# Optimization experiments

Hardware: AMD Instinct MI355X
Metric: run time of the kernel (lower is better)

## Reference

```python
import jax, jax.numpy as jnp
import numpy as np

LN_EPS = 1e-5
NEG_SLOPE = 0.01  # torch LeakyReLU default


def layernorm(x, w, b):
    m = jnp.mean(x, axis=-1, keepdims=True)
    v = jnp.mean((x - m) ** 2, axis=-1, keepdims=True)
    return (x - m) * jax.lax.rsqrt(v + LN_EPS) * w + b


def setup_inputs() -> dict:
    key = jax.random.key(0)
    ks = jax.random.split(key, 12)
    B, T, C, E = 16, 1024, 768, 2
    d = C
    s = 0.02
    inp = {
        "x": jax.random.normal(ks[0], (B, T, C), jnp.float32),
        "ln1_w": jnp.ones((C,), jnp.float32),
        "ln1_b": jnp.zeros((C,), jnp.float32),
        "wqkv": jax.random.normal(ks[1], (C, 3 * C), jnp.float32) * s,
        "bqkv": jnp.zeros((3 * C,), jnp.float32),
        "wproj": jax.random.normal(ks[2], (C, C), jnp.float32) * s,
        "bproj": jnp.zeros((C,), jnp.float32),
        "ln2_w": jnp.ones((C,), jnp.float32),
        "ln2_b": jnp.zeros((C,), jnp.float32),
        "wg": jax.random.normal(ks[3], (C, E), jnp.float32) * s,
        # Experts module uses torch.randn (std 1); we scale down for numerics
        "w1": jax.random.normal(ks[4], (E, d, 4 * d), jnp.float32) * s,
        "w2": jax.random.normal(ks[5], (E, 4 * d, 4 * d), jnp.float32) * s,
        "w3": jax.random.normal(ks[6], (E, 4 * d, d), jnp.float32) * s,
        "n_head": 12,
    }
    return inp


def block_forward(x, ln1_w, ln1_b, wqkv, bqkv, wproj, bproj,
                  ln2_w, ln2_b, wg, w1, w2, w3, n_head):
    B, T, C = x.shape
    H = n_head
    hd = C // H
    E = wg.shape[-1]

    # ---- causal self-attention + residual ----
    h = layernorm(x, ln1_w, ln1_b)
    qkv = h @ wqkv + bqkv                      # [B,T,3C]
    q, k, v = jnp.split(qkv, 3, axis=-1)
    q = q.reshape(B, T, H, hd).transpose(0, 2, 1, 3)  # bhtd
    k = k.reshape(B, T, H, hd).transpose(0, 2, 1, 3)
    v = v.reshape(B, T, H, hd).transpose(0, 2, 1, 3)
    scores = jnp.einsum('bhqd,bhkd->bhqk', q, k) / jnp.sqrt(jnp.float32(hd))
    causal = jnp.tril(jnp.ones((T, T), bool))
    scores = jnp.where(causal, scores, jnp.finfo(scores.dtype).min)
    attn = jax.nn.softmax(scores, axis=-1)
    y = jnp.einsum('bhqk,bhkd->bhqd', attn, v)
    y = y.transpose(0, 2, 1, 3).reshape(B, T, C)
    x = x + (y @ wproj + bproj)

    # ---- MoE (top-2 gating, capacity dispatch) + residual ----
    h2 = layernorm(x, ln2_w, ln2_b)
    capacity = (T * 2) // E                    # capacity_factor = 1.0, top-2
    raw_gates = jax.nn.softmax(h2 @ wg, axis=-1)   # [B,T,E]

    idx1 = jnp.argmax(raw_gates, axis=-1)
    mask1 = jax.nn.one_hot(idx1, E, dtype=raw_gates.dtype)
    gate1 = jnp.sum(raw_gates * mask1, axis=-1)    # [B,T]
    gates2 = raw_gates * (1.0 - mask1)
    idx2 = jnp.argmax(gates2, axis=-1)
    mask2 = jax.nn.one_hot(idx2, E, dtype=raw_gates.dtype)
    gate2 = jnp.sum(raw_gates * mask2, axis=-1)
    denom = gate1 + gate2 + 1e-9
    gate1, gate2 = gate1 / denom, gate2 / denom

    # aux load-balancing loss (before capacity truncation)
    density = jnp.mean(mask1, axis=1)              # [B,E]
    density_proxy = jnp.mean(raw_gates, axis=1)    # [B,E]
    aux_loss = jnp.mean(density * density_proxy) * (E * E)

    # positions within each expert buffer (exclusive cumsum over tokens)
    pos1 = jnp.cumsum(mask1, axis=1) - mask1       # [B,T,E]
    mask1 = mask1 * (pos1 < capacity)
    mask1_count = jnp.sum(mask1, axis=1, keepdims=True)
    pos2 = (jnp.cumsum(mask2, axis=1) - mask2) + mask1_count
    mask2 = mask2 * (pos2 < capacity)

    oh1 = jax.nn.one_hot(pos1.astype(jnp.int32), capacity, dtype=raw_gates.dtype)
    oh2 = jax.nn.one_hot(pos2.astype(jnp.int32), capacity, dtype=raw_gates.dtype)
    combine = (gate1[..., None] * mask1)[..., None] * oh1 \
            + (gate2[..., None] * mask2)[..., None] * oh2   # [B,T,E,C]
    dispatch = (combine > 0).astype(h2.dtype)

    # dispatch -> per-expert batches
    expert_in = jnp.einsum('bnd,bnec->ebcd', h2, dispatch)   # [E,B,Cap,d]
    Bc = B * capacity
    ei = expert_in.reshape(E, Bc, C)
    lrelu = lambda z: jnp.where(z >= 0, z, NEG_SLOPE * z)
    hh = lrelu(jnp.einsum('end,edh->enh', ei, w1))
    hh = lrelu(jnp.einsum('end,edh->enh', hh, w2))
    eo = jnp.einsum('end,edh->enh', hh, w3).reshape(E, B, capacity, C)
    moe_out = jnp.einsum('ebcd,bnec->bnd', eo, combine)

    x = x + moe_out
    return x, aux_loss


def reference(x, ln1_w, ln1_b, wqkv, bqkv, wproj, bproj,
              ln2_w, ln2_b, wg, w1, w2, w3, n_head):
    return block_forward(x, ln1_w, ln1_b, wqkv, bqkv, wproj, bproj,
                         ln2_w, ln2_b, wg, w1, w2, w3, n_head)
```

## Files before the change

### kernel.cpp

```cpp
#include <hip/hip_runtime.h>
#include <cstdint>
#include <cstddef>

constexpr int B_  = 16;
constexpr int T_  = 1024;
constexpr int C_  = 768;
constexpr int H_  = 12;
constexpr int HD_ = 64;
constexpr int BT_ = B_ * T_;
constexpr int C3_ = 3 * C_;
constexpr int FF_ = 4 * C_;
constexpr int MCH_ = 8192;

typedef __bf16 bf16x8 __attribute__((ext_vector_type(8)));
typedef float  floatx4 __attribute__((ext_vector_type(4)));
typedef unsigned short u16x8 __attribute__((ext_vector_type(8)));

__device__ inline float bf2f(unsigned short u) {
  union { unsigned int i; float f; } x; x.i = ((unsigned int)u) << 16; return x.f;
}
__device__ inline unsigned short f2bf(float f) {
  union { float f; unsigned int i; } x; x.f = f;
  unsigned int u = x.i;
  u += 0x7fffu + ((u >> 16) & 1u);
  return (unsigned short)(u >> 16);
}

#define GLOAD_LDS16(gp, lp)                                              \
  __builtin_amdgcn_global_load_lds(                                      \
      (__attribute__((address_space(1))) void*)(gp),                     \
      (__attribute__((address_space(3))) void*)(lp), 16, 0, 0)

__launch_bounds__(256)
__global__ void ln_kernel(const float* __restrict__ x, const float* __restrict__ w,
                          const float* __restrict__ b, unsigned short* __restrict__ out) {
  int row = blockIdx.x;
  int tid = threadIdx.x;
  const float* xr = x + (size_t)row * C_;
  float v0 = xr[tid], v1 = xr[tid + 256], v2 = xr[tid + 512];
  float s  = v0 + v1 + v2;
  float ss = v0 * v0 + v1 * v1 + v2 * v2;
#pragma unroll
  for (int off = 32; off > 0; off >>= 1) {
    s  += __shfl_down(s, off, 64);
    ss += __shfl_down(ss, off, 64);
  }
  __shared__ float red[8];
  int wid = tid >> 6;
  if ((tid & 63) == 0) { red[wid] = s; red[4 + wid] = ss; }
  __syncthreads();
  float st  = red[0] + red[1] + red[2] + red[3];
  float sst = red[4] + red[5] + red[6] + red[7];
  float mean = st * (1.0f / C_);
  float var  = sst * (1.0f / C_) - mean * mean;
  float rstd = rsqrtf(var + 1e-5f);
  unsigned short* orow = out + (size_t)row * C_;
  orow[tid]       = f2bf((v0 - mean) * rstd * w[tid]       + b[tid]);
  orow[tid + 256] = f2bf((v1 - mean) * rstd * w[tid + 256] + b[tid + 256]);
  orow[tid + 512] = f2bf((v2 - mean) * rstd * w[tid + 512] + b[tid + 512]);
}

__launch_bounds__(256)
__global__ void convT(const float* __restrict__ in, unsigned short* __restrict__ out,
                      int K, int N) {
  __shared__ float t[32][33];
  int n0 = blockIdx.x * 32, k0 = blockIdx.y * 32;
  int tx = threadIdx.x & 31, ty = threadIdx.x >> 5;
#pragma unroll
  for (int r = 0; r < 32; r += 8)
    t[r + ty][tx] = in[(size_t)(k0 + r + ty) * N + n0 + tx];
  __syncthreads();
#pragma unroll
  for (int r = 0; r < 32; r += 8)
    out[(size_t)(n0 + r + ty) * K + k0 + tx] = f2bf(t[tx][r + ty]);
}

template <int ACT, bool BIAS, bool RES, bool COMBINE, bool OUTBF16>
__launch_bounds__(256)
__global__ void gemm_bf16(const unsigned short* __restrict__ A,
                          const unsigned short* __restrict__ Bt,
                          const float* __restrict__ bias,
                          const float* __restrict__ Rres,
                          const float* __restrict__ gates2, int eidx,
                          void* __restrict__ Cout,
                          int M, int N, int K) {
  __shared__ __attribute__((aligned(16))) unsigned short Als[8192];
  __shared__ __attribute__((aligned(16))) unsigned short Bls[8192];
  const int tid  = threadIdx.x;
  const int wave = tid >> 6, lane = tid & 63;
  const int wr = wave >> 1, wc = wave & 1;
  const int m0 = blockIdx.y * 128, n0 = blockIdx.x * 128;

  const int srow = wave * 32 + (lane >> 3);
  const int skg  = (lane & 7) ^ ((lane >> 3) & 7);
  const unsigned short* Ap = A  + (size_t)(m0 + srow) * K + skg * 8;
  const unsigned short* Bp = Bt + (size_t)(n0 + srow) * K + skg * 8;
  unsigned short* AlsW = Als + wave * 2048;
  unsigned short* BlsW = Bls + wave * 2048;

  floatx4 acc[4][4];
#pragma unroll
  for (int i = 0; i < 4; ++i)
#pragma unroll
    for (int j = 0; j < 4; ++j) acc[i][j] = floatx4{0.f, 0.f, 0.f, 0.f};

  const int q  = lane >> 4;
  const int ml = lane & 15;
  const int rsw = ml & 7;

  for (int k0 = 0; k0 < K; k0 += 64) {
    __syncthreads();
#pragma unroll
    for (int i = 0; i < 4; ++i) {
      GLOAD_LDS16(Ap + (size_t)(i * 8) * K + k0, AlsW + i * 512);
      GLOAD_LDS16(Bp + (size_t)(i * 8) * K + k0, BlsW + i * 512);
    }
    __syncthreads();
#pragma unroll
    for (int ks = 0; ks < 2; ++ks) {
      const int p = (ks * 4 + q) ^ rsw;
      bf16x8 af[4], bfg[4];
#pragma unroll
      for (int i = 0; i < 4; ++i) {
        int ar = wr * 64 + i * 16 + ml;
        af[i]  = *(const bf16x8*)&Als[(ar * 8 + p) * 8];
        int br = wc * 64 + i * 16 + ml;
        bfg[i] = *(const bf16x8*)&Bls[(br * 8 + p) * 8];
      }
#pragma unroll
      for (int i = 0; i < 4; ++i)
#pragma unroll
        for (int j = 0; j < 4; ++j)
          acc[i][j] = __builtin_amdgcn_mfma_f32_16x16x32_bf16(af[i], bfg[j], acc[i][j], 0, 0, 0);
    }
  }

  const int rbase = q * 4;
#pragma unroll
  for (int i = 0; i < 4; ++i) {
    int row = m0 + wr * 64 + i * 16 + rbase;
#pragma unroll
    for (int j = 0; j < 4; ++j) {
      int col = n0 + wc * 64 + j * 16 + ml;
      float bcol = BIAS ? bias[col] : 0.f;
#pragma unroll
      for (int r = 0; r < 4; ++r) {
        float v = acc[i][j][r];
        if (BIAS) v += bcol;
        if (ACT == 1) v = (v >= 0.f) ? v : 0.01f * v;
        if (RES) v += Rres[(size_t)(row + r) * N + col];
        if (COMBINE) {
          float g = gates2[2 * (row + r) + eidx];
          float* op = (float*)Cout + (size_t)(row + r) * N + col;
          *op += g * v;
        } else if (OUTBF16) {
          ((unsigned short*)Cout)[(size_t)(row + r) * N + col] = f2bf(v);
        } else {
          ((float*)Cout)[(size_t)(row + r) * N + col] = v;
        }
      }
    }
  }
}

__launch_bounds__(256)
__global__ void attn_kernel(const unsigned short* __restrict__ qkv,
                            unsigned short* __restrict__ y) {
  __shared__ __attribute__((aligned(16))) unsigned short Qls[64 * 64];
  __shared__ __attribute__((aligned(16))) unsigned short Kls[64 * 64];
  __shared__ __attribute__((aligned(16))) unsigned short Vt[64 * 72];
  __shared__ __attribute__((aligned(16))) unsigned short Pls[4 * 16 * 72];

  const int tid  = threadIdx.x;
  const int wave = tid >> 6, lane = tid & 63;
  const int quad = lane >> 4, n = lane & 15;
  const int q0 = blockIdx.x * 64;
  const int bh = blockIdx.y;
  const int b = bh / H_, h = bh % H_;
  const size_t base = (size_t)b * T_ * C3_ + (size_t)h * HD_;

  {
    const int r8 = lane >> 3;
    const int g  = (lane & 7) ^ r8;
#pragma unroll
    for (int i = 0; i < 2; ++i) {
      int row = wave * 16 + i * 8 + r8;
      GLOAD_LDS16(qkv + base + (size_t)(q0 + row) * C3_ + g * 8,
                  Qls + wave * 1024 + i * 512);
    }
  }

  floatx4 O[4];
#pragma unroll
  for (int ct = 0; ct < 4; ++ct) O[ct] = floatx4{0.f, 0.f, 0.f, 0.f};
  float mrow[4] = {-1e30f, -1e30f, -1e30f, -1e30f};
  float lrow[4] = {0.f, 0.f, 0.f, 0.f};

  const int nkt = blockIdx.x + 1;
  unsigned short* Pw = Pls + wave * (16 * 72);

  for (int kt = 0; kt < nkt; ++kt) {
    const int k0 = kt << 6;
    __syncthreads();
    {
      const int r8 = lane >> 3;
      const int g  = (lane & 7) ^ r8;
#pragma unroll
      for (int i = 0; i < 2; ++i) {
        int key = wave * 16 + i * 8 + r8;
        GLOAD_LDS16(qkv + base + (size_t)(k0 + key) * C3_ + C_ + g * 8,
                    Kls + wave * 1024 + i * 512);
      }
    }
    {
      int key = tid & 63;
      int dbase = (tid >> 6) * 8;
#pragma unroll
      for (int it = 0; it < 2; ++it) {
        int d0 = dbase + it * 32;
        u16x8 vv = *(const u16x8*)(qkv + base + (size_t)(k0 + key) * C3_ + 2 * C_ + d0);
#pragma unroll
        for (int j = 0; j < 8; ++j) Vt[(d0 + j) * 72 + key] = vv[j];
      }
    }
    __syncthreads();

    floatx4 sacc[4];
#pragma unroll
    for (int ct = 0; ct < 4; ++ct) sacc[ct] = floatx4{0.f, 0.f, 0.f, 0.f};
#pragma unroll
    for (int ks = 0; ks < 2; ++ks) {
      const int ga = (ks * 4 + quad) ^ (n & 7);
      bf16x8 aq = *(const bf16x8*)&Qls[((wave * 16 + n) * 8 + ga) * 8];
#pragma unroll
      for (int ct = 0; ct < 4; ++ct) {
        bf16x8 kb = *(const bf16x8*)&Kls[((ct * 16 + n) * 8 + ga) * 8];
        sacc[ct] = __builtin_amdgcn_mfma_f32_16x16x32_bf16(aq, kb, sacc[ct], 0, 0, 0);
      }
    }

    float p[4][4];
#pragma unroll
    for (int ct = 0; ct < 4; ++ct)
#pragma unroll
      for (int r = 0; r < 4; ++r) p[ct][r] = sacc[ct][r] * 0.125f;
    if (kt == nkt - 1) {
      const int kgb = k0 + n, qgb = q0 + wave * 16 + quad * 4;
#pragma unroll
      for (int ct = 0; ct < 4; ++ct)
#pragma unroll
        for (int r = 0; r < 4; ++r)
          if (kgb + ct * 16 > qgb + r) p[ct][r] = -1e30f;
    }
#pragma unroll
    for (int r = 0; r < 4; ++r) {
      float tm = fmaxf(fmaxf(p[0][r], p[1][r]), fmaxf(p[2][r], p[3][r]));
      tm = fmaxf(tm, __shfl_xor(tm, 1, 64));
      tm = fmaxf(tm, __shfl_xor(tm, 2, 64));
      tm = fmaxf(tm, __shfl_xor(tm, 4, 64));
      tm = fmaxf(tm, __shfl_xor(tm, 8, 64));
      float mn = fmaxf(mrow[r], tm);
      float alpha = __expf(mrow[r] - mn);
      mrow[r] = mn;
      float ps = 0.f;
#pragma unroll
      for (int ct = 0; ct < 4; ++ct) {
        float pe = __expf(p[ct][r] - mn);
        p[ct][r] = pe;
        ps += pe;
      }
      ps += __shfl_xor(ps, 1, 64);
      ps += __shfl_xor(ps, 2, 64);
      ps += __shfl_xor(ps, 4, 64);
      ps += __shfl_xor(ps, 8, 64);
      lrow[r] = lrow[r] * alpha + ps;
      O[0][r] *= alpha; O[1][r] *= alpha; O[2][r] *= alpha; O[3][r] *= alpha;
    }

#pragma unroll
    for (int ct = 0; ct < 4; ++ct)
#pragma unroll
      for (int r = 0; r < 4; ++r)
        Pw[(quad * 4 + r) * 72 + ct * 16 + n] = f2bf(p[ct][r]);

#pragma unroll
    for (int ks = 0; ks < 2; ++ks) {
      bf16x8 pa = *(const bf16x8*)&Pw[n * 72 + (ks * 4 + quad) * 8];
#pragma unroll
      for (int ct = 0; ct < 4; ++ct) {
        bf16x8 vb = *(const bf16x8*)&Vt[(ct * 16 + n) * 72 + (ks * 4 + quad) * 8];
        O[ct] = __builtin_amdgcn_mfma_f32_16x16x32_bf16(pa, vb, O[ct], 0, 0, 0);
      }
    }
  }

#pragma unroll
  for (int r = 0; r < 4; ++r) {
    float inv = 1.0f / lrow[r];
    int row = q0 + wave * 16 + quad * 4 + r;
    unsigned short* dst = y + ((size_t)b * T_ + row) * C_ + h * HD_;
#pragma unroll
    for (int ct = 0; ct < 4; ++ct)
      dst[ct * 16 + n] = f2bf(O[ct][r] * inv);
  }
}

__launch_bounds__(256)
__global__ void gate_kernel(const unsigned short* __restrict__ h2,
                            const float* __restrict__ wg,
                            float* __restrict__ gates) {
  int wave = threadIdx.x >> 6, lane = threadIdx.x & 63;
  int t = blockIdx.x * 4 + wave;
  const unsigned short* hr = h2 + (size_t)t * C_;
  float a0 = 0.0f, a1 = 0.0f;
#pragma unroll
  for (int i = 0; i < 12; ++i) {
    int d = lane + 64 * i;
    float hv = bf2f(hr[d]);
    a0 += hv * wg[2 * d];
    a1 += hv * wg[2 * d + 1];
  }
#pragma unroll
  for (int off = 32; off > 0; off >>= 1) {
    a0 += __shfl_down(a0, off, 64);
    a1 += __shfl_down(a1, off, 64);
  }
  if (lane == 0) {
    float m  = fmaxf(a0, a1);
    float e0 = __expf(a0 - m), e1 = __expf(a1 - m);
    float invs = 1.0f / (e0 + e1);
    float p0 = e0 * invs, p1 = e1 * invs;
    const float gnorm = 1.0f / (1.0f + 1e-9f);
    gates[2 * t]     = p0 * gnorm;
    gates[2 * t + 1] = p1 * gnorm;
  }
}

__launch_bounds__(1024)
__global__ void moe_stats_kernel(const float* __restrict__ gates,
                                 float* __restrict__ out_aux) {
  int wave = threadIdx.x >> 6, lane = threadIdx.x & 63;
  float c0 = 0.f, sp0 = 0.f, sp1 = 0.f;
#pragma unroll
  for (int j = 0; j < 16; ++j) {
    int t = wave * T_ + lane + 64 * j;
    float p0 = gates[2 * t], p1 = gates[2 * t + 1];
    c0  += (p1 > p0) ? 0.f : 1.f;
    sp0 += p0;
    sp1 += p1;
  }
#pragma unroll
  for (int off = 32; off > 0; off >>= 1) {
    c0  += __shfl_down(c0, off, 64);
    sp0 += __shfl_down(sp0, off, 64);
    sp1 += __shfl_down(sp1, off, 64);
  }
  __shared__ float red[16][3];
  if (lane == 0) { red[wave][0] = c0; red[wave][1] = sp0; red[wave][2] = sp1; }
  __syncthreads();
  if (threadIdx.x == 0) {
    float s = 0.f;
    for (int b = 0; b < B_; ++b) {
      float cc0 = red[b][0];
      float d0 = cc0 * (1.f / T_), d1 = (T_ - cc0) * (1.f / T_);
      float px0 = red[b][1] * (1.f / T_), px1 = red[b][2] * (1.f / T_);
      s += d0 * px0 + d1 * px1;
    }
    out_aux[0] = s * (4.f / 32.f);
  }
}

extern "C" void kernel_launch(void* const* d_in, const int* in_sizes, int n_in,
                              void* d_out, int out_size, void* d_ws, size_t ws_size,
                              hipStream_t stream) {
  const float* x     = (const float*)d_in[0];
  const float* ln1_w = (const float*)d_in[1];
  const float* ln1_b = (const float*)d_in[2];
  const float* wqkv  = (const float*)d_in[3];
  const float* bqkv  = (const float*)d_in[4];
  const float* wproj = (const float*)d_in[5];
  const float* bproj = (const float*)d_in[6];
  const float* ln2_w = (const float*)d_in[7];
  const float* ln2_b = (const float*)d_in[8];
  const float* wg    = (const float*)d_in[9];
  const float* w1    = (const float*)d_in[10];
  const float* w2    = (const float*)d_in[11];
  const float* w3    = (const float*)d_in[12];
  float* out = (float*)d_out;

  unsigned short* wsu   = (unsigned short*)d_ws;
  unsigned short* wqkvT = wsu;
  unsigned short* wprojT= wqkvT + (size_t)C3_ * C_;
  unsigned short* w1T   = wprojT + (size_t)C_ * C_;
  unsigned short* w2T   = w1T + (size_t)2 * FF_ * C_;
  unsigned short* w3T   = w2T + (size_t)2 * FF_ * FF_;
  unsigned short* hb    = w3T + (size_t)2 * C_ * FF_;
  unsigned short* region= hb + (size_t)BT_ * C_;
  unsigned short* qkvb  = region;
  unsigned short* yb    = region + (size_t)BT_ * C3_;
  unsigned short* hh1   = region;
  unsigned short* hh2   = region + (size_t)MCH_ * FF_;
  float* gates = (float*)(region + (size_t)BT_ * 4 * C_);

  convT<<<dim3(C3_ / 32, C_ / 32), 256, 0, stream>>>(wqkv, wqkvT, C_, C3_);
  convT<<<dim3(C_ / 32, C_ / 32), 256, 0, stream>>>(wproj, wprojT, C_, C_);
  for (int e = 0; e < 2; ++e) {
    convT<<<dim3(FF_ / 32, C_ / 32), 256, 0, stream>>>(
        w1 + (size_t)e * C_ * FF_, w1T + (size_t)e * FF_ * C_, C_, FF_);
    convT<<<dim3(FF_ / 32, FF_ / 32), 256, 0, stream>>>(
        w2 + (size_t)e * FF_ * FF_, w2T + (size_t)e * FF_ * FF_, FF_, FF_);
    convT<<<dim3(C_ / 32, FF_ / 32), 256, 0, stream>>>(
        w3 + (size_t)e * FF_ * C_, w3T + (size_t)e * C_ * FF_, FF_, C_);
  }

  ln_kernel<<<BT_, 256, 0, stream>>>(x, ln1_w, ln1_b, hb);
  gemm_bf16<0, true, false, false, true><<<dim3(C3_ / 128, BT_ / 128), 256, 0, stream>>>(
      hb, wqkvT, bqkv, nullptr, nullptr, 0, qkvb, BT_, C3_, C_);
  attn_kernel<<<dim3(T_ / 64, B_ * H_), 256, 0, stream>>>(qkvb, yb);
  gemm_bf16<0, true, true, false, false><<<dim3(C_ / 128, BT_ / 128), 256, 0, stream>>>(
      yb, wprojT, bproj, x, nullptr, 0, out, BT_, C_, C_);

  ln_kernel<<<BT_, 256, 0, stream>>>(out, ln2_w, ln2_b, hb);
  gate_kernel<<<BT_ / 4, 256, 0, stream>>>(hb, wg, gates);
  moe_stats_kernel<<<1, 1024, 0, stream>>>(gates, out + (size_t)BT_ * C_);

  for (int e = 0; e < 2; ++e) {
    for (int c = 0; c < BT_ / MCH_; ++c) {
      const unsigned short* a = hb + (size_t)c * MCH_ * C_;
      gemm_bf16<1, false, false, false, true><<<dim3(FF_ / 128, MCH_ / 128), 256, 0, stream>>>(
          a, w1T + (size_t)e * FF_ * C_, nullptr, nullptr, nullptr, 0, hh1, MCH_, FF_, C_);
      gemm_bf16<1, false, false, false, true><<<dim3(FF_ / 128, MCH_ / 128), 256, 0, stream>>>(
          hh1, w2T + (size_t)e * FF_ * FF_, nullptr, nullptr, nullptr, 0, hh2, MCH_, FF_, FF_);
      gemm_bf16<0, false, false, true, false><<<dim3(C_ / 128, MCH_ / 128), 256, 0, stream>>>(
          hh2, w3T + (size_t)e * C_ * FF_, nullptr, nullptr,
          gates + (size_t)2 * c * MCH_, e, out + (size_t)c * MCH_ * C_, MCH_, C_, FF_);
    }
  }
}
```

Baseline: 1.781 ms.

## Batch weight transposes, swizzle GEMM tiles, pre-transpose V, double-buffer attention

All weight conversion launches are merged into one batched transpose kernel. The GEMM gets an XCD-style block index swizzle for better L2 locality. The QKV GEMM epilogue writes V transposed into a separate buffer so attention can load V with async global-to-LDS copies. K/V tiles in attention are double-buffered so the next tile's loads overlap compute. The transposed V store is strided and uncoalesced, and the new double-buffered pipeline drops a sync, which risks an LDS race.

```diff
diff --git a/kernel.cpp b/kernel.cpp
--- a/kernel.cpp
+++ b/kernel.cpp
@@ -9,6 +9,7 @@
 constexpr int HD_ = 64;
 constexpr int BT_ = B_ * T_;
 constexpr int C3_ = 3 * C_;
+constexpr int QK2_ = 2 * C_;
 constexpr int FF_ = 4 * C_;
 constexpr int MCH_ = 8192;
 
@@ -60,12 +61,27 @@
   orow[tid + 512] = f2bf((v2 - mean) * rstd * w[tid + 512] + b[tid + 512]);
 }
 
+struct CtJobs {
+  const float* in[8];
+  unsigned short* out[8];
+  int K[8], N[8], tX[8];
+  int t0[9];
+};
+
 __launch_bounds__(256)
-__global__ void convT(const float* __restrict__ in, unsigned short* __restrict__ out,
-                      int K, int N) {
+__global__ void convT_batch(CtJobs J) {
   __shared__ float t[32][33];
-  int n0 = blockIdx.x * 32, k0 = blockIdx.y * 32;
-  int tx = threadIdx.x & 31, ty = threadIdx.x >> 5;
+  int bid = blockIdx.x;
+  int ji = 0;
+#pragma unroll
+  for (int i = 0; i < 7; ++i) ji += (bid >= J.t0[i + 1]) ? 1 : 0;
+  const float* in = J.in[ji];
+  unsigned short* out = J.out[ji];
+  const int K = J.K[ji], N = J.N[ji];
+  const int lt = bid - J.t0[ji];
+  const int bx = lt % J.tX[ji], by = lt / J.tX[ji];
+  const int n0 = bx * 32, k0 = by * 32;
+  const int tx = threadIdx.x & 31, ty = threadIdx.x >> 5;
 #pragma unroll
   for (int r = 0; r < 32; r += 8)
     t[r + ty][tx] = in[(size_t)(k0 + r + ty) * N + n0 + tx];
@@ -75,7 +91,7 @@
     out[(size_t)(n0 + r + ty) * K + k0 + tx] = f2bf(t[tx][r + ty]);
 }
 
-template <int ACT, bool BIAS, bool RES, bool COMBINE, bool OUTBF16>
+template <int ACT, bool BIAS, bool RES, bool COMBINE, bool OUTBF16, bool VSPLIT = false>
 __launch_bounds__(256)
 __global__ void gemm_bf16(const unsigned short* __restrict__ A,
                           const unsigned short* __restrict__ Bt,
@@ -83,13 +99,25 @@
                           const float* __restrict__ Rres,
                           const float* __restrict__ gates2, int eidx,
                           void* __restrict__ Cout,
+                          unsigned short* __restrict__ vtout,
                           int M, int N, int K) {
   __shared__ __attribute__((aligned(16))) unsigned short Als[8192];
   __shared__ __attribute__((aligned(16))) unsigned short Bls[8192];
   const int tid  = threadIdx.x;
   const int wave = tid >> 6, lane = tid & 63;
   const int wr = wave >> 1, wc = wave & 1;
-  const int m0 = blockIdx.y * 128, n0 = blockIdx.x * 128;
+
+  int bx = blockIdx.x, by = blockIdx.y;
+  {
+    const int nbx = gridDim.x;
+    const int nwg = nbx * gridDim.y;
+    if ((nwg & 7) == 0) {
+      const int bid = by * nbx + bx;
+      const int swz = (bid & 7) * (nwg >> 3) + (bid >> 3);
+      by = swz / nbx; bx = swz - by * nbx;
+    }
+  }
+  const int m0 = by * 128, n0 = bx * 128;
 
   const int srow = wave * 32 + (lane >> 3);
   const int skg  = (lane & 7) ^ ((lane >> 3) & 7);
@@ -153,6 +181,12 @@
           float g = gates2[2 * (row + r) + eidx];
           float* op = (float*)Cout + (size_t)(row + r) * N + col;
           *op += g * v;
+        } else if (VSPLIT) {
+          if (col < QK2_) {
+            ((unsigned short*)Cout)[(size_t)(row + r) * QK2_ + col] = f2bf(v);
+          } else {
+            vtout[(size_t)(col - QK2_) * BT_ + row + r] = f2bf(v);
+          }
         } else if (OUTBF16) {
           ((unsigned short*)Cout)[(size_t)(row + r) * N + col] = f2bf(v);
         } else {
@@ -164,11 +198,12 @@
 }
 
 __launch_bounds__(256)
-__global__ void attn_kernel(const unsigned short* __restrict__ qkv,
+__global__ void attn_kernel(const unsigned short* __restrict__ qk,
+                            const unsigned short* __restrict__ vT,
                             unsigned short* __restrict__ y) {
   __shared__ __attribute__((aligned(16))) unsigned short Qls[64 * 64];
-  __shared__ __attribute__((aligned(16))) unsigned short Kls[64 * 64];
-  __shared__ __attribute__((aligned(16))) unsigned short Vt[64 * 72];
+  __shared__ __attribute__((aligned(16))) unsigned short K2[2][64 * 64];
+  __shared__ __attribute__((aligned(16))) unsigned short V2[2][64 * 64];
   __shared__ __attribute__((aligned(16))) unsigned short Pls[4 * 16 * 72];
 
   const int tid  = threadIdx.x;
@@ -177,18 +212,32 @@
   const int q0 = blockIdx.x * 64;
   const int bh = blockIdx.y;
   const int b = bh / H_, h = bh % H_;
-  const size_t base = (size_t)b * T_ * C3_ + (size_t)h * HD_;
-
-  {
-    const int r8 = lane >> 3;
-    const int g  = (lane & 7) ^ r8;
-#pragma unroll
-    for (int i = 0; i < 2; ++i) {
-      int row = wave * 16 + i * 8 + r8;
-      GLOAD_LDS16(qkv + base + (size_t)(q0 + row) * C3_ + g * 8,
-                  Qls + wave * 1024 + i * 512);
-    }
-  }
+  const size_t qbase = (size_t)b * T_ * QK2_ + (size_t)h * HD_;
+  const size_t vbase = (size_t)h * HD_ * BT_ + (size_t)b * T_;
+
+  const int r8 = lane >> 3;
+  const int g  = (lane & 7) ^ r8;
+
+#pragma unroll
+  for (int i = 0; i < 2; ++i) {
+    int row = wave * 16 + i * 8 + r8;
+    GLOAD_LDS16(qk + qbase + (size_t)(q0 + row) * QK2_ + g * 8,
+                Qls + wave * 1024 + i * 512);
+  }
+
+#define STAGE_KV(bf, k0)                                                      \
+  do {                                                                        \
+    _Pragma("unroll")                                                         \
+    for (int i = 0; i < 2; ++i) {                                             \
+      int row = wave * 16 + i * 8 + r8;                                       \
+      GLOAD_LDS16(qk + qbase + (size_t)((k0) + row) * QK2_ + C_ + g * 8,      \
+                  K2[bf] + wave * 1024 + i * 512);                            \
+      GLOAD_LDS16(vT + vbase + (size_t)row * BT_ + (k0) + g * 8,              \
+                  V2[bf] + wave * 1024 + i * 512);                            \
+    }                                                                         \
+  } while (0)
+
+  STAGE_KV(0, 0);
 
   floatx4 O[4];
 #pragma unroll
@@ -200,30 +249,9 @@
   unsigned short* Pw = Pls + wave * (16 * 72);
 
   for (int kt = 0; kt < nkt; ++kt) {
-    const int k0 = kt << 6;
+    const int cur = kt & 1;
     __syncthreads();
-    {
-      const int r8 = lane >> 3;
-      const int g  = (lane & 7) ^ r8;
-#pragma unroll
-      for (int i = 0; i < 2; ++i) {
-        int key = wave * 16 + i * 8 + r8;
-        GLOAD_LDS16(qkv + base + (size_t)(k0 + key) * C3_ + C_ + g * 8,
-                    Kls + wave * 1024 + i * 512);
-      }
-    }
-    {
-      int key = tid & 63;
-      int dbase = (tid >> 6) * 8;
-#pragma unroll
-      for (int it = 0; it < 2; ++it) {
-        int d0 = dbase + it * 32;
-        u16x8 vv = *(const u16x8*)(qkv + base + (size_t)(k0 + key) * C3_ + 2 * C_ + d0);
-#pragma unroll
-        for (int j = 0; j < 8; ++j) Vt[(d0 + j) * 72 + key] = vv[j];
-      }
-    }
-    __syncthreads();
+    if (kt + 1 < nkt) STAGE_KV(cur ^ 1, (kt + 1) << 6);
 
     floatx4 sacc[4];
 #pragma unroll
@@ -234,7 +262,7 @@
       bf16x8 aq = *(const bf16x8*)&Qls[((wave * 16 + n) * 8 + ga) * 8];
 #pragma unroll
       for (int ct = 0; ct < 4; ++ct) {
-        bf16x8 kb = *(const bf16x8*)&Kls[((ct * 16 + n) * 8 + ga) * 8];
+        bf16x8 kb = *(const bf16x8*)&K2[cur][((ct * 16 + n) * 8 + ga) * 8];
         sacc[ct] = __builtin_amdgcn_mfma_f32_16x16x32_bf16(aq, kb, sacc[ct], 0, 0, 0);
       }
     }
@@ -245,7 +273,7 @@
 #pragma unroll
       for (int r = 0; r < 4; ++r) p[ct][r] = sacc[ct][r] * 0.125f;
     if (kt == nkt - 1) {
-      const int kgb = k0 + n, qgb = q0 + wave * 16 + quad * 4;
+      const int kgb = (kt << 6) + n, qgb = q0 + wave * 16 + quad * 4;
 #pragma unroll
       for (int ct = 0; ct < 4; ++ct)
 #pragma unroll
@@ -286,9 +314,10 @@
 #pragma unroll
     for (int ks = 0; ks < 2; ++ks) {
       bf16x8 pa = *(const bf16x8*)&Pw[n * 72 + (ks * 4 + quad) * 8];
+      const int gv = (ks * 4 + quad) ^ (n & 7);
 #pragma unroll
       for (int ct = 0; ct < 4; ++ct) {
-        bf16x8 vb = *(const bf16x8*)&Vt[(ct * 16 + n) * 72 + (ks * 4 + quad) * 8];
+        bf16x8 vb = *(const bf16x8*)&V2[cur][((ct * 16 + n) * 8 + gv) * 8];
         O[ct] = __builtin_amdgcn_mfma_f32_16x16x32_bf16(pa, vb, O[ct], 0, 0, 0);
       }
     }
@@ -303,6 +332,7 @@
     for (int ct = 0; ct < 4; ++ct)
       dst[ct * 16 + n] = f2bf(O[ct][r] * inv);
   }
+#undef STAGE_KV
 }
 
 __launch_bounds__(256)
@@ -396,29 +426,39 @@
   unsigned short* w3T   = w2T + (size_t)2 * FF_ * FF_;
   unsigned short* hb    = w3T + (size_t)2 * C_ * FF_;
   unsigned short* region= hb + (size_t)BT_ * C_;
-  unsigned short* qkvb  = region;
-  unsigned short* yb    = region + (size_t)BT_ * C3_;
+  unsigned short* qkb   = region;
+  unsigned short* vTb   = region + (size_t)BT_ * QK2_;
+  unsigned short* yb    = region + (size_t)BT_ * 3 * C_;
   unsigned short* hh1   = region;
   unsigned short* hh2   = region + (size_t)MCH_ * FF_;
   float* gates = (float*)(region + (size_t)BT_ * 4 * C_);
 
-  convT<<<dim3(C3_ / 32, C_ / 32), 256, 0, stream>>>(wqkv, wqkvT, C_, C3_);
-  convT<<<dim3(C_ / 32, C_ / 32), 256, 0, stream>>>(wproj, wprojT, C_, C_);
-  for (int e = 0; e < 2; ++e) {
-    convT<<<dim3(FF_ / 32, C_ / 32), 256, 0, stream>>>(
-        w1 + (size_t)e * C_ * FF_, w1T + (size_t)e * FF_ * C_, C_, FF_);
-    convT<<<dim3(FF_ / 32, FF_ / 32), 256, 0, stream>>>(
-        w2 + (size_t)e * FF_ * FF_, w2T + (size_t)e * FF_ * FF_, FF_, FF_);
-    convT<<<dim3(C_ / 32, FF_ / 32), 256, 0, stream>>>(
-        w3 + (size_t)e * FF_ * C_, w3T + (size_t)e * C_ * FF_, FF_, C_);
+  {
+    CtJobs J;
+    int idx = 0, acc = 0;
+    auto add = [&](const float* in, unsigned short* outp, int K, int N) {
+      J.in[idx] = in; J.out[idx] = outp; J.K[idx] = K; J.N[idx] = N;
+      J.tX[idx] = N / 32; J.t0[idx] = acc;
+      acc += (N / 32) * (K / 32);
+      ++idx;
+    };
+    add(wqkv, wqkvT, C_, C3_);
+    add(wproj, wprojT, C_, C_);
+    for (int e = 0; e < 2; ++e) {
+      add(w1 + (size_t)e * C_ * FF_, w1T + (size_t)e * FF_ * C_, C_, FF_);
+      add(w2 + (size_t)e * FF_ * FF_, w2T + (size_t)e * FF_ * FF_, FF_, FF_);
+      add(w3 + (size_t)e * FF_ * C_, w3T + (size_t)e * C_ * FF_, FF_, C_);
+    }
+    J.t0[8] = acc;
+    convT_batch<<<acc, 256, 0, stream>>>(J);
   }
 
   ln_kernel<<<BT_, 256, 0, stream>>>(x, ln1_w, ln1_b, hb);
-  gemm_bf16<0, true, false, false, true><<<dim3(C3_ / 128, BT_ / 128), 256, 0, stream>>>(
-      hb, wqkvT, bqkv, nullptr, nullptr, 0, qkvb, BT_, C3_, C_);
-  attn_kernel<<<dim3(T_ / 64, B_ * H_), 256, 0, stream>>>(qkvb, yb);
+  gemm_bf16<0, true, false, false, true, true><<<dim3(C3_ / 128, BT_ / 128), 256, 0, stream>>>(
+      hb, wqkvT, bqkv, nullptr, nullptr, 0, qkb, vTb, BT_, C3_, C_);
+  attn_kernel<<<dim3(T_ / 64, B_ * H_), 256, 0, stream>>>(qkb, vTb, yb);
   gemm_bf16<0, true, true, false, false><<<dim3(C_ / 128, BT_ / 128), 256, 0, stream>>>(
-      yb, wprojT, bproj, x, nullptr, 0, out, BT_, C_, C_);
+      yb, wprojT, bproj, x, nullptr, 0, out, nullptr, BT_, C_, C_);
 
   ln_kernel<<<BT_, 256, 0, stream>>>(out, ln2_w, ln2_b, hb);
   gate_kernel<<<BT_ / 4, 256, 0, stream>>>(hb, wg, gates);
@@ -428,12 +468,12 @@
     for (int c = 0; c < BT_ / MCH_; ++c) {
       const unsigned short* a = hb + (size_t)c * MCH_ * C_;
       gemm_bf16<1, false, false, false, true><<<dim3(FF_ / 128, MCH_ / 128), 256, 0, stream>>>(
-          a, w1T + (size_t)e * FF_ * C_, nullptr, nullptr, nullptr, 0, hh1, MCH_, FF_, C_);
+          a, w1T + (size_t)e * FF_ * C_, nullptr, nullptr, nullptr, 0, hh1, nullptr, MCH_, FF_, C_);
       gemm_bf16<1, false, false, false, true><<<dim3(FF_ / 128, MCH_ / 128), 256, 0, stream>>>(
-          hh1, w2T + (size_t)e * FF_ * FF_, nullptr, nullptr, nullptr, 0, hh2, MCH_, FF_, FF_);
+          hh1, w2T + (size_t)e * FF_ * FF_, nullptr, nullptr, nullptr, 0, hh2, nullptr, MCH_, FF_, FF_);
       gemm_bf16<0, false, false, true, false><<<dim3(C_ / 128, MCH_ / 128), 256, 0, stream>>>(
           hh2, w3T + (size_t)e * C_ * FF_, nullptr, nullptr,
-          gates + (size_t)2 * c * MCH_, e, out + (size_t)c * MCH_ * C_, MCH_, C_, FF_);
-    }
-  }
-}
+          gates + (size_t)2 * c * MCH_, e, out + (size_t)c * MCH_ * C_, nullptr, MCH_, C_, FF_);
+    }
+  }
+}
```

Result: no change. 1.761 ms (-1.1%).
